# Kernel tuning notes

Hardware: AMD Instinct MI355X
Metric: run time of the kernel (lower is better)

The kernel has to match this reference:

```python
import jax, jax.numpy as jnp
import numpy as np

B, T, N, IN = 16, 12, 2048, 1
HID, E_DIM, CHEB, HOR = 64, 10, 2, 12


def setup_inputs() -> dict:
    key = jax.random.key(0)
    ks = jax.random.split(key, 12)
    s = 0.1  # param scale to keep gates unsaturated
    return {
        "source": jax.random.normal(ks[0], (B, T, N, IN), jnp.float32),
        "node_embeddings": jax.random.normal(ks[1], (N, E_DIM), jnp.float32),
        "Wg0": jax.random.normal(ks[2], (E_DIM, CHEB, IN + HID, 2 * HID), jnp.float32) * s,
        "bg0": jax.random.normal(ks[3], (E_DIM, 2 * HID), jnp.float32) * s,
        "Wu0": jax.random.normal(ks[4], (E_DIM, CHEB, IN + HID, HID), jnp.float32) * s,
        "bu0": jax.random.normal(ks[5], (E_DIM, HID), jnp.float32) * s,
        "Wg1": jax.random.normal(ks[6], (E_DIM, CHEB, HID + HID, 2 * HID), jnp.float32) * s,
        "bg1": jax.random.normal(ks[7], (E_DIM, 2 * HID), jnp.float32) * s,
        "Wu1": jax.random.normal(ks[8], (E_DIM, CHEB, HID + HID, HID), jnp.float32) * s,
        "bu1": jax.random.normal(ks[9], (E_DIM, HID), jnp.float32) * s,
        "conv_w": jax.random.normal(ks[10], (HOR, HID), jnp.float32) * s,
        "conv_b": jax.random.normal(ks[11], (HOR,), jnp.float32) * s,
    }


def _cheb_supports(E, cheb_k):
    # softmax(relu(E E^T)) row-normalized adaptive adjacency + Chebyshev recursion
    S = jax.nn.softmax(jax.nn.relu(E @ E.T), axis=1)
    sup = [jnp.eye(E.shape[0], dtype=S.dtype), S]
    for _ in range(2, cheb_k):
        sup.append(2.0 * S @ sup[-1] - sup[-2])
    return jnp.stack(sup, axis=0)  # (K, N, N)


def _gcn(x, supports, weights, bias):
    # x: (B,N,C); weights: (N,K,C,O); bias: (N,O)
    x_g = jnp.einsum('knm,bmc->bnkc', supports, x)
    return jnp.einsum('bnki,nkio->bno', x_g, weights) + bias


def _layer(x_seq, supports, E, Wg, bg, Wu, bu, hid):
    # precompute node-adaptive weights/biases (constant across time)
    wg = jnp.einsum('nd,dkio->nkio', E, Wg)
    bgv = E @ bg
    wu = jnp.einsum('nd,dkio->nkio', E, Wu)
    buv = E @ bu

    def step(state, x_t):
        inp = jnp.concatenate([x_t, state], axis=-1)
        zr = jax.nn.sigmoid(_gcn(inp, supports, wg, bgv))
        z, r = jnp.split(zr, 2, axis=-1)
        cand = jnp.concatenate([x_t, z * state], axis=-1)
        hc = jnp.tanh(_gcn(cand, supports, wu, buv))
        h = r * state + (1.0 - r) * hc
        return h, h

    init = jnp.zeros((x_seq.shape[0], x_seq.shape[2], hid), dtype=x_seq.dtype)
    _, hs = jax.lax.scan(step, init, jnp.swapaxes(x_seq, 0, 1))  # (T,B,N,H)
    return jnp.swapaxes(hs, 0, 1)  # (B,T,N,H)


def reference(source, node_embeddings, Wg0, bg0, Wu0, bu0, Wg1, bg1, Wu1, bu1, conv_w, conv_b):
    supports = _cheb_supports(node_embeddings, CHEB)
    h1 = _layer(source, supports, node_embeddings, Wg0, bg0, Wu0, bu0, HID)
    h2 = _layer(h1, supports, node_embeddings, Wg1, bg1, Wu1, bu1, HID)
    last = h2[:, -1]  # (B,N,HID)
    # Conv2d(1, horizon, kernel=(1,HID)) on (B,1,N,HID) == per-node linear over HID
    out = jnp.einsum('bnc,hc->bhn', last, conv_w) + conv_b[None, :, None]
    return out  # (B, horizon, N)
```

## Files before the change

kernel.cpp:

```cpp
#include <hip/hip_runtime.h>
#include <hip/hip_bf16.h>


#define B_    16
#define T_    12
#define N_    2048
#define HID_  64
#define ED_   10
#define HOR_  12
#define BH    (B_*HID_)
#define BT    (B_*T_)

typedef __hip_bfloat16 bf16;
typedef __attribute__((ext_vector_type(8))) short short8;
typedef __attribute__((ext_vector_type(4))) float floatx4;

__device__ __forceinline__ float b2f(bf16 x){ return __bfloat162float(x); }
__device__ __forceinline__ bf16  f2b(float x){ return __float2bfloat16(x); }
__device__ __forceinline__ float bits2f(unsigned u) {
  union { float f; unsigned i; } c; c.i = u << 16; return c.f;
}
__device__ __forceinline__ float ldin(const void* p, size_t i, int isbf) {
  return isbf ? b2f(((const bf16*)p)[i]) : ((const float*)p)[i];
}
__device__ __forceinline__ void fma4(float4& a, float s, const float4& b) {
  a.x += s*b.x; a.y += s*b.y; a.z += s*b.z; a.w += s*b.w;
}

__global__ void k_detect(const void* __restrict__ E, int* __restrict__ flag) {
  __shared__ int cnt;
  if (threadIdx.x == 0) cnt = 0;
  __syncthreads();
  const unsigned* w = (const unsigned*)E;
  int c = 0;
  for (int i = threadIdx.x; i < 4096; i += 256) {
    const unsigned e = (w[i] >> 7) & 0xFFu;
    if (e >= 0x6Eu && e <= 0x86u) ++c;
  }
  atomicAdd(&cnt, c);
  __syncthreads();
  if (threadIdx.x == 0) flag[0] = (cnt > 2048) ? 1 : 0;
}

__global__ void k_castE(const void* __restrict__ E, float* __restrict__ Ein,
                        const int* __restrict__ flag) {
  const int i = blockIdx.x*256 + threadIdx.x;
  if (i < N_*ED_) Ein[i] = ldin(E, i, flag[0]);
}
__global__ void k_castsrc(const void* __restrict__ src, float* __restrict__ srcf,
                          const int* __restrict__ flag) {
  const int i = blockIdx.x*256 + threadIdx.x;
  if (i < B_*T_*N_) srcf[i] = ldin(src, i, flag[0]);
}
__global__ void k_castc(const void* __restrict__ cw, const void* __restrict__ cb,
                        float* __restrict__ cwf, float* __restrict__ cbf,
                        const int* __restrict__ flag) {
  const int i = blockIdx.x*256 + threadIdx.x;
  const int f = flag[0];
  if (i < HOR_*HID_) cwf[i] = ldin(cw, i, f);
  if (i < HOR_)      cbf[i] = ldin(cb, i, f);
}

__global__ __launch_bounds__(256) void k_softmax_S(const float* __restrict__ Ein,
                                                   float* __restrict__ S) {
  const int n = blockIdx.x, tid = threadIdx.x;
  __shared__ float er[ED_];
  __shared__ float red[4];
  if (tid < ED_) er[tid] = Ein[n*ED_ + tid];
  __syncthreads();
  float e[ED_];
#pragma unroll
  for (int d = 0; d < ED_; ++d) e[d] = er[d];
  float v[8];
  float mx = 0.f;
#pragma unroll
  for (int j = 0; j < 8; ++j) {
    const int m = tid + j*256;
    float dot = 0.f;
#pragma unroll
    for (int d = 0; d < ED_; ++d) dot += e[d]*Ein[m*ED_ + d];
    v[j] = fmaxf(dot, 0.f);
    mx = fmaxf(mx, v[j]);
  }
  for (int o = 32; o; o >>= 1) mx = fmaxf(mx, __shfl_xor(mx, o, 64));
  if ((tid & 63) == 0) red[tid >> 6] = mx;
  __syncthreads();
  mx = fmaxf(fmaxf(red[0], red[1]), fmaxf(red[2], red[3]));
  __syncthreads();
  float sum = 0.f;
#pragma unroll
  for (int j = 0; j < 8; ++j) { v[j] = __expf(v[j] - mx); sum += v[j]; }
  for (int o = 32; o; o >>= 1) sum += __shfl_xor(sum, o, 64);
  if ((tid & 63) == 0) red[tid >> 6] = sum;
  __syncthreads();
  sum = red[0] + red[1] + red[2] + red[3];
  const float inv = 1.f / sum;
#pragma unroll
  for (int j = 0; j < 8; ++j)
    S[(size_t)n*N_ + tid + j*256] = v[j]*inv;
}

__global__ void k_splitS(const float* __restrict__ S, bf16* __restrict__ Sh,
                         bf16* __restrict__ Sl, int n) {
  const int i = blockIdx.x*256 + threadIdx.x;
  if (i < n) {
    const float v = S[i];
    const bf16 h = f2b(v);
    Sh[i] = h;
    Sl[i] = f2b(v - b2f(h));
  }
}

template<int LAYER>
__global__ __launch_bounds__(256) void k_prepP(const void* __restrict__ Wb,
                                               float* __restrict__ PF,
                                               bf16* __restrict__ PH,
                                               int KIin, int KIP, int O,
                                               const int* __restrict__ flag) {
  const int idx = blockIdx.x*256 + threadIdx.x;
  if (idx >= ED_*O*KIP) return;
  const int d = idx / (O*KIP), rem = idx - d*O*KIP;
  const int o = rem / KIP, kp = rem - o*KIP;
  int cheb, i; bool valid;
  if (LAYER == 0) {
    cheb = (kp >= 80) ? 1 : 0;
    const int local = kp - cheb*80;
    if (local < 64)       { i = local + 1; valid = true; }
    else if (local == 64) { i = 0;         valid = true; }
    else                  { i = 0;         valid = false; }
  } else {
    cheb = kp >> 7; i = kp & 127; valid = true;
  }
  float v = 0.f;
  if (valid) v = ldin(Wb, (size_t)((d*2 + cheb)*KIin + i)*O + o, flag[0]);
  const int kg = kp >> 2, e = kp & 3;
  const size_t pi = ((size_t)(o*(KIP/4) + kg)*ED_ + d)*4 + e;
  PF[pi] = v;
  PH[pi] = f2b(v);
}

__global__ __launch_bounds__(128) void k_matb(const float* __restrict__ Ein,
                                              const void* __restrict__ bb,
                                              float* __restrict__ outv, int O,
                                              const int* __restrict__ flag) {
  const int n = blockIdx.x, tid = threadIdx.x;
  if (tid >= O) return;
  const int f = flag[0];
  float acc = 0.f;
#pragma unroll
  for (int d = 0; d < ED_; ++d) acc += Ein[n*ED_ + d]*ldin(bb, d*O + tid, f);
  outv[n*O + tid] = acc;
}

__global__ __launch_bounds__(256) void k_gemm64T(const float* __restrict__ S,
                                                 const float* __restrict__ X,
                                                 float* __restrict__ C,
                                                 int ldx, int ldc) {
  const int bm = blockIdx.x * 64;
  const int bc = blockIdx.y * 64;
  __shared__ float St[64][68];
  __shared__ float Xt[64][68];
  const int tid = threadIdx.x;
  const int r0 = (tid >> 4) * 4;
  const int c0 = (tid & 15) * 4;
  float acc[4][4];
#pragma unroll
  for (int i = 0; i < 4; ++i)
#pragma unroll
    for (int j = 0; j < 4; ++j) acc[i][j] = 0.f;
  for (int mk = 0; mk < N_; mk += 64) {
    {
      const int r = tid >> 2, ks = (tid & 3) * 16;
      const float* sp = S + (size_t)(bm + r)*N_ + mk + ks;
#pragma unroll
      for (int u = 0; u < 16; ++u) St[ks + u][r] = sp[u];
      const float* xp = X + (size_t)(bc + r)*ldx + mk + ks;
#pragma unroll
      for (int u = 0; u < 16; ++u) Xt[ks + u][r] = xp[u];
    }
    __syncthreads();
#pragma unroll 4
    for (int kk = 0; kk < 64; ++kk) {
      const float a0 = St[kk][r0], a1 = St[kk][r0+1],
                  a2 = St[kk][r0+2], a3 = St[kk][r0+3];
      const float b0 = Xt[kk][c0], b1 = Xt[kk][c0+1],
                  b2 = Xt[kk][c0+2], b3 = Xt[kk][c0+3];
      acc[0][0] += a0*b0; acc[0][1] += a0*b1; acc[0][2] += a0*b2; acc[0][3] += a0*b3;
      acc[1][0] += a1*b0; acc[1][1] += a1*b1; acc[1][2] += a1*b2; acc[1][3] += a1*b3;
      acc[2][0] += a2*b0; acc[2][1] += a2*b1; acc[2][2] += a2*b2; acc[2][3] += a2*b3;
      acc[3][0] += a3*b0; acc[3][1] += a3*b1; acc[3][2] += a3*b2; acc[3][3] += a3*b3;
    }
    __syncthreads();
  }
#pragma unroll
  for (int i = 0; i < 4; ++i)
#pragma unroll
    for (int j = 0; j < 4; ++j)
      C[(size_t)(bm + r0 + i)*ldc + bc + c0 + j] = acc[i][j];
}

__global__ __launch_bounds__(256) void k_gemmM(const bf16* __restrict__ Sh,
                                               const bf16* __restrict__ Sl,
                                               const bf16* __restrict__ X1h,
                                               const bf16* __restrict__ X1l,
                                               float* __restrict__ C1, int ldc1,
                                               const bf16* __restrict__ X2h,
                                               const bf16* __restrict__ X2l,
                                               float* __restrict__ C2, int ldc2,
                                               int split) {
  const int bm = blockIdx.x * 128;
  int bc = blockIdx.y * 64;
  const bf16* Xh = X1h; const bf16* Xl = X1l; float* C = C1; int ldc = ldc1;
  if (bc >= split) { Xh = X2h; Xl = X2l; C = C2; ldc = ldc2; bc -= split; }

  __shared__ __align__(16) bf16 Ah[128][72];
  __shared__ __align__(16) bf16 Al[128][72];
  __shared__ __align__(16) bf16 Bh[64][72];
  __shared__ __align__(16) bf16 Bl[64][72];
  const int tid = threadIdx.x;
  const int wave = tid >> 6, lane = tid & 63, q = lane >> 4, ln = lane & 15;
  const int wm = wave >> 1, wn = wave & 1;
  const int srow = tid >> 3, scol = (tid & 7) * 8;

  floatx4 acc[4][2];
#pragma unroll
  for (int mt = 0; mt < 4; ++mt)
#pragma unroll
    for (int nt = 0; nt < 2; ++nt) acc[mt][nt] = (floatx4){0.f,0.f,0.f,0.f};

  for (int mk = 0; mk < N_; mk += 64) {
#pragma unroll
    for (int i = 0; i < 4; ++i) {
      const int r = i*32 + srow;
      *(uint4*)&Ah[r][scol] = *(const uint4*)(Sh + (size_t)(bm + r)*N_ + mk + scol);
      *(uint4*)&Al[r][scol] = *(const uint4*)(Sl + (size_t)(bm + r)*N_ + mk + scol);
    }
#pragma unroll
    for (int i = 0; i < 2; ++i) {
      const int r = i*32 + srow;
      *(uint4*)&Bh[r][scol] = *(const uint4*)(Xh + (size_t)(bc + r)*N_ + mk + scol);
      *(uint4*)&Bl[r][scol] = *(const uint4*)(Xl + (size_t)(bc + r)*N_ + mk + scol);
    }
    __syncthreads();
#pragma unroll
    for (int ks = 0; ks < 64; ks += 32) {
      short8 ah[4], al[4], bh[2], bl[2];
#pragma unroll
      for (int mt = 0; mt < 4; ++mt) {
        ah[mt] = *(const short8*)&Ah[wm*64 + mt*16 + ln][ks + q*8];
        al[mt] = *(const short8*)&Al[wm*64 + mt*16 + ln][ks + q*8];
      }
#pragma unroll
      for (int nt = 0; nt < 2; ++nt) {
        bh[nt] = *(const short8*)&Bh[wn*32 + nt*16 + ln][ks + q*8];
        bl[nt] = *(const short8*)&Bl[wn*32 + nt*16 + ln][ks + q*8];
      }
#pragma unroll
      for (int mt = 0; mt < 4; ++mt)
#pragma unroll
        for (int nt = 0; nt < 2; ++nt) {
          acc[mt][nt] = __builtin_amdgcn_mfma_f32_16x16x32_bf16(ah[mt], bh[nt], acc[mt][nt], 0, 0, 0);
          acc[mt][nt] = __builtin_amdgcn_mfma_f32_16x16x32_bf16(al[mt], bh[nt], acc[mt][nt], 0, 0, 0);
          acc[mt][nt] = __builtin_amdgcn_mfma_f32_16x16x32_bf16(ah[mt], bl[nt], acc[mt][nt], 0, 0, 0);
        }
    }
    __syncthreads();
  }
#pragma unroll
  for (int mt = 0; mt < 4; ++mt)
#pragma unroll
    for (int nt = 0; nt < 2; ++nt)
#pragma unroll
      for (int r = 0; r < 4; ++r)
        C[(size_t)(bm + wm*64 + mt*16 + q*4 + r)*ldc + bc + wn*32 + nt*16 + ln] =
            acc[mt][nt][r];
}

template<int LAYER, int KIP, int KIPP>
__device__ __forceinline__ void build4(float (*xg)[KIPP],
                                       const float* p0, const float* p1,
                                       const float* p2, const float* p3,
                                       int n, int t, int tid) {
  constexpr int NQ = KIP/4;
  for (int idx = tid; idx < B_*NQ; idx += 256) {
    const int b = idx / NQ, k = (idx - b*NQ) * 4;
    float4 v = make_float4(0.f, 0.f, 0.f, 0.f);
    if (LAYER == 1) {
      const float* rg = (k < 64) ? p0 : (k < 128) ? p1 : (k < 192) ? p2 : p3;
      v = *(const float4*)(rg + (size_t)n*BH + b*64 + (k & 63));
    } else {
      if (k < 64)        v = *(const float4*)(p0 + (size_t)n*BH + b*64 + k);
      else if (k == 64)  v.x = p1[(size_t)(b*T_ + t)*N_ + n];
      else if (k >= 80 && k < 144)
                         v = *(const float4*)(p2 + (size_t)n*BH + b*64 + (k - 80));
      else if (k == 144) v.x = p3[(size_t)n*BT + b*T_ + t];
    }
    *(float4*)&xg[b][k] = v;
  }
}

template<int KIP>
__device__ __forceinline__ float4 merge_p(const float* __restrict__ PF,
                                          const bf16* __restrict__ PH,
                                          const float* el, int o, int kg,
                                          int isbf) {
  float4 a4 = make_float4(0.f, 0.f, 0.f, 0.f);
  const size_t gbase = (size_t)(o*(KIP/4) + kg)*(ED_*4);
  if (isbf) {
    const uint4* g = (const uint4*)(PH + gbase);
#pragma unroll
    for (int i = 0; i < 5; ++i) {
      const uint4 w = g[i];
      const float e0 = el[2*i], e1 = el[2*i + 1];
      a4.x += e0*bits2f(w.x & 0xFFFFu); a4.y += e0*bits2f(w.x >> 16);
      a4.z += e0*bits2f(w.y & 0xFFFFu); a4.w += e0*bits2f(w.y >> 16);
      a4.x += e1*bits2f(w.z & 0xFFFFu); a4.y += e1*bits2f(w.z >> 16);
      a4.z += e1*bits2f(w.w & 0xFFFFu); a4.w += e1*bits2f(w.w >> 16);
    }
  } else {
    const float4* g = (const float4*)(PF + gbase);
#pragma unroll
    for (int d = 0; d < ED_; ++d)
      fma4(a4, el[d], g[d]);
  }
  return a4;
}

template<int KIP>
__device__ __forceinline__ void merge_p2(const float* __restrict__ PF,
                                         const bf16* __restrict__ PH,
                                         const float* el0, const float* el1,
                                         int o, int kg, int isbf,
                                         float4& a0, float4& a1) {
  const size_t gbase = (size_t)(o*(KIP/4) + kg)*(ED_*4);
  if (isbf) {
    const uint4* g = (const uint4*)(PH + gbase);
#pragma unroll
    for (int i = 0; i < 5; ++i) {
      const uint4 w = g[i];
      const float f0 = bits2f(w.x & 0xFFFFu), f1 = bits2f(w.x >> 16);
      const float f2 = bits2f(w.y & 0xFFFFu), f3 = bits2f(w.y >> 16);
      const float f4 = bits2f(w.z & 0xFFFFu), f5 = bits2f(w.z >> 16);
      const float f6 = bits2f(w.w & 0xFFFFu), f7 = bits2f(w.w >> 16);
      const float e00 = el0[2*i], e01 = el0[2*i + 1];
      const float e10 = el1[2*i], e11 = el1[2*i + 1];
      a0.x += e00*f0; a0.y += e00*f1; a0.z += e00*f2; a0.w += e00*f3;
      a0.x += e01*f4; a0.y += e01*f5; a0.z += e01*f6; a0.w += e01*f7;
      a1.x += e10*f0; a1.y += e10*f1; a1.z += e10*f2; a1.w += e10*f3;
      a1.x += e11*f4; a1.y += e11*f5; a1.z += e11*f6; a1.w += e11*f7;
    }
  } else {
    const float4* g = (const float4*)(PF + gbase);
#pragma unroll
    for (int d = 0; d < ED_; ++d) {
      const float4 w = g[d];
      fma4(a0, el0[d], w);
      fma4(a1, el1[d], w);
    }
  }
}

template<int KIP>
__global__ __launch_bounds__(256) void k_merge(const float* __restrict__ PF,
                                               const bf16* __restrict__ PH,
                                               const float* __restrict__ Ein,
                                               float* __restrict__ WM, int O,
                                               const int* __restrict__ flag) {
  const int n = blockIdx.x;
  const int idx = blockIdx.y*256 + threadIdx.x;
  __shared__ float es[ED_];
  if (threadIdx.x < ED_) es[threadIdx.x] = Ein[n*ED_ + threadIdx.x];
  __syncthreads();
  if (idx >= O*(KIP/4)) return;
  const int o = idx / (KIP/4), kg = idx - o*(KIP/4);
  float el[ED_];
#pragma unroll
  for (int d = 0; d < ED_; ++d) el[d] = es[d];
  const float4 a4 = merge_p<KIP>(PF, PH, el, o, kg, flag[0]);
  *(float4*)&WM[((size_t)n*O + o)*KIP + kg*4] = a4;
}

template<int LAYER, int KIP>
__global__ __launch_bounds__(256, 2) void k_gateWpm(const float* __restrict__ WM,
                                                    const float* __restrict__ bgv,
                                                    const float* __restrict__ p0,
                                                    const float* __restrict__ p1,
                                                    const float* __restrict__ p2,
                                                    const float* __restrict__ p3,
                                                    const float* __restrict__ hstate,
                                                    float* __restrict__ zh,
                                                    bf16* __restrict__ zhTh,
                                                    bf16* __restrict__ zhTl,
                                                    float* __restrict__ r_buf,
                                                    int t) {
  constexpr int KIPP = KIP + 4;
  constexpr int O = 128;
  const int n = blockIdx.x, tid = threadIdx.x;
  __shared__ float xg[B_][KIPP];
  __shared__ float wm[O][36];
  build4<LAYER, KIP, KIPP>(xg, p0, p1, p2, p3, n, t, tid);

  const float* WMn = WM + (size_t)n*O*KIP;
  const int b = tid >> 4, q = tid & 15;
  float acc[8];
#pragma unroll
  for (int j = 0; j < 8; ++j) acc[j] = 0.f;

  for (int k0 = 0; k0 < KIP; k0 += 32) {
#pragma unroll
    for (int i = 0; i < O*8/256; ++i) {
      const int idx = tid + i*256;
      const int o = idx >> 3, kq = idx & 7;
      *(float4*)&wm[o][kq*4] =
          *(const float4*)(WMn + (size_t)o*KIP + k0 + kq*4);
    }
    __syncthreads();
#pragma unroll
    for (int kq = 0; kq < 8; ++kq) {
      const float4 xv = *(const float4*)&xg[b][k0 + kq*4];
#pragma unroll
      for (int j = 0; j < 8; ++j) {
        const float4 wv = *(const float4*)&wm[q + 16*j][kq*4];
        acc[j] += xv.x*wv.x + xv.y*wv.y + xv.z*wv.z + xv.w*wv.w;
      }
    }
    __syncthreads();
  }
#pragma unroll
  for (int j = 0; j < 8; ++j) {
    const int o = q + 16*j;
    float s = acc[j] + bgv[n*128 + o];
    s = 1.f/(1.f + __expf(-s));
    if (o < HID_) {
      const float zv = s*hstate[(size_t)n*BH + b*64 + o];
      zh[(size_t)n*BH + b*64 + o] = zv;
      const bf16 h = f2b(zv);
      zhTh[(size_t)(b*64 + o)*N_ + n] = h;
      zhTl[(size_t)(b*64 + o)*N_ + n] = f2b(zv - b2f(h));
    } else {
      r_buf[(size_t)n*BH + b*64 + (o - HID_)] = s;
    }
  }
}

template<int LAYER, int KIP>
__global__ __launch_bounds__(256, 2) void k_candWpm(const float* __restrict__ WM,
                                                    const float* __restrict__ buv,
                                                    const float* __restrict__ p0,
                                                    const float* __restrict__ p1,
                                                    const float* __restrict__ p2,
                                                    const float* __restrict__ p3,
                                                    const float* __restrict__ r_buf,
                                                    float* __restrict__ hstate,
                                                    bf16* __restrict__ hTh,
                                                    bf16* __restrict__ hTl,
                                                    int t) {
  constexpr int KIPP = KIP + 4;
  constexpr int O = 64;
  const int n = blockIdx.x, tid = threadIdx.x;
  __shared__ float xg[B_][KIPP];
  __shared__ float wm[O][36];
  build4<LAYER, KIP, KIPP>(xg, p0, p1, p2, p3, n, t, tid);

  const float* WMn = WM + (size_t)n*O*KIP;
  const int b = tid >> 4, q = tid & 15;
  float acc[4];
#pragma unroll
  for (int j = 0; j < 4; ++j) acc[j] = 0.f;

  for (int k0 = 0; k0 < KIP; k0 += 32) {
#pragma unroll
    for (int i = 0; i < O*8/256; ++i) {
      const int idx = tid + i*256;
      const int o = idx >> 3, kq = idx & 7;
      *(float4*)&wm[o][kq*4] =
          *(const float4*)(WMn + (size_t)o*KIP + k0 + kq*4);
    }
    __syncthreads();
#pragma unroll
    for (int kq = 0; kq < 8; ++kq) {
      const float4 xv = *(const float4*)&xg[b][k0 + kq*4];
#pragma unroll
      for (int j = 0; j < 4; ++j) {
        const float4 wv = *(const float4*)&wm[q + 16*j][kq*4];
        acc[j] += xv.x*wv.x + xv.y*wv.y + xv.z*wv.z + xv.w*wv.w;
      }
    }
    __syncthreads();
  }
#pragma unroll
  for (int j = 0; j < 4; ++j) {
    const int o = q + 16*j;
    const float hc = tanhf(acc[j] + buv[n*64 + o]);
    const float rr = r_buf[(size_t)n*BH + b*64 + o];
    const float hold = hstate[(size_t)n*BH + b*64 + o];
    const float hn = rr*hold + (1.f - rr)*hc;
    hstate[(size_t)n*BH + b*64 + o] = hn;
    const bf16 h = f2b(hn);
    hTh[(size_t)(b*64 + o)*N_ + n] = h;
    hTl[(size_t)(b*64 + o)*N_ + n] = f2b(hn - b2f(h));
  }
}

template<int LAYER, int KIP>
__global__ __launch_bounds__(256) void k_gateW(const float* __restrict__ PF,
                                               const bf16* __restrict__ PH,
                                               const float* __restrict__ bgv,
                                               const float* __restrict__ p0,
                                               const float* __restrict__ p1,
                                               const float* __restrict__ p2,
                                               const float* __restrict__ p3,
                                               const float* __restrict__ Ein,
                                               const float* __restrict__ hstate,
                                               float* __restrict__ zh,
                                               bf16* __restrict__ zhTh,
                                               bf16* __restrict__ zhTl,
                                               float* __restrict__ r_buf,
                                               const int* __restrict__ flag,
                                               int t) {
  constexpr int KIPP = KIP + 4;
  constexpr int O = 128;
  const int n = blockIdx.x, tid = threadIdx.x;
  __shared__ float xg[B_][KIPP];
  __shared__ float wm[O][36];
  __shared__ float es[ED_];
  if (tid < ED_) es[tid] = Ein[n*ED_ + tid];
  build4<LAYER, KIP, KIPP>(xg, p0, p1, p2, p3, n, t, tid);
  __syncthreads();
  const int isbf = flag[0];
  float el[ED_];
#pragma unroll
  for (int d = 0; d < ED_; ++d) el[d] = es[d];

  const int b = tid >> 4, q = tid & 15;
  float acc[8];
#pragma unroll
  for (int j = 0; j < 8; ++j) acc[j] = 0.f;

  for (int k0 = 0; k0 < KIP; k0 += 32) {
#pragma unroll
    for (int i = 0; i < O*8/256; ++i) {
      const int idx = tid + i*256;
      const int o = idx >> 3, kq = idx & 7;
      const float4 a4 = merge_p<KIP>(PF, PH, el, o, (k0 >> 2) + kq, isbf);
      *(float4*)&wm[o][kq*4] = a4;
    }
    __syncthreads();
#pragma unroll
    for (int kq = 0; kq < 8; ++kq) {
      const float4 xv = *(const float4*)&xg[b][k0 + kq*4];
#pragma unroll
      for (int j = 0; j < 8; ++j) {
        const float4 wv = *(const float4*)&wm[q + 16*j][kq*4];
        acc[j] += xv.x*wv.x + xv.y*wv.y + xv.z*wv.z + xv.w*wv.w;
      }
    }
    __syncthreads();
  }
#pragma unroll
  for (int j = 0; j < 8; ++j) {
    const int o = q + 16*j;
    float s = acc[j] + bgv[n*128 + o];
    s = 1.f/(1.f + __expf(-s));
    if (o < HID_) {
      const float zv = s*hstate[(size_t)n*BH + b*64 + o];
      zh[(size_t)n*BH + b*64 + o] = zv;
      const bf16 h = f2b(zv);
      zhTh[(size_t)(b*64 + o)*N_ + n] = h;
      zhTl[(size_t)(b*64 + o)*N_ + n] = f2b(zv - b2f(h));
    } else {
      r_buf[(size_t)n*BH + b*64 + (o - HID_)] = s;
    }
  }
}

template<int LAYER, int KIP>
__global__ __launch_bounds__(256, 2) void k_gateW2(const float* __restrict__ PF,
                                                   const bf16* __restrict__ PH,
                                                   const float* __restrict__ bgv,
                                                   const float* __restrict__ p0,
                                                   const float* __restrict__ p1,
                                                   const float* __restrict__ p2,
                                                   const float* __restrict__ p3,
                                                   const float* __restrict__ Ein,
                                                   const float* __restrict__ hstate,
                                                   float* __restrict__ zh,
                                                   bf16* __restrict__ zhTh,
                                                   bf16* __restrict__ zhTl,
                                                   float* __restrict__ r_buf,
                                                   const int* __restrict__ flag,
                                                   int t) {
  constexpr int KIPP = KIP + 4;
  constexpr int O = 128;
  const int n0 = blockIdx.x, n1 = blockIdx.x + N_/2, tid = threadIdx.x;
  __shared__ float xg[2][B_][KIPP];
  __shared__ float wm[2][O][36];
  __shared__ float es[2][ED_];
  if (tid < ED_) es[0][tid] = Ein[n0*ED_ + tid];
  if (tid >= 32 && tid < 32 + ED_) es[1][tid - 32] = Ein[n1*ED_ + (tid - 32)];
  build4<LAYER, KIP, KIPP>(xg[0], p0, p1, p2, p3, n0, t, tid);
  build4<LAYER, KIP, KIPP>(xg[1], p0, p1, p2, p3, n1, t, tid);
  __syncthreads();
  const int isbf = flag[0];
  float el0[ED_], el1[ED_];
#pragma unroll
  for (int d = 0; d < ED_; ++d) { el0[d] = es[0][d]; el1[d] = es[1][d]; }

  const int b = tid >> 4, q = tid & 15;
  float ac0[8], ac1[8];
#pragma unroll
  for (int j = 0; j < 8; ++j) { ac0[j] = 0.f; ac1[j] = 0.f; }

  for (int k0 = 0; k0 < KIP; k0 += 32) {
#pragma unroll
    for (int i = 0; i < O*8/256; ++i) {
      const int idx = tid + i*256;
      const int o = idx >> 3, kq = idx & 7;
      float4 a0 = make_float4(0.f, 0.f, 0.f, 0.f);
      float4 a1 = make_float4(0.f, 0.f, 0.f, 0.f);
      merge_p2<KIP>(PF, PH, el0, el1, o, (k0 >> 2) + kq, isbf, a0, a1);
      *(float4*)&wm[0][o][kq*4] = a0;
      *(float4*)&wm[1][o][kq*4] = a1;
    }
    __syncthreads();
#pragma unroll
    for (int kq = 0; kq < 8; ++kq) {
      const float4 xv0 = *(const float4*)&xg[0][b][k0 + kq*4];
      const float4 xv1 = *(const float4*)&xg[1][b][k0 + kq*4];
#pragma unroll
      for (int j = 0; j < 8; ++j) {
        const float4 w0 = *(const float4*)&wm[0][q + 16*j][kq*4];
        const float4 w1 = *(const float4*)&wm[1][q + 16*j][kq*4];
        ac0[j] += xv0.x*w0.x + xv0.y*w0.y + xv0.z*w0.z + xv0.w*w0.w;
        ac1[j] += xv1.x*w1.x + xv1.y*w1.y + xv1.z*w1.z + xv1.w*w1.w;
      }
    }
    __syncthreads();
  }
#pragma unroll
  for (int j = 0; j < 8; ++j) {
    const int o = q + 16*j;
    {
      float s = ac0[j] + bgv[n0*128 + o];
      s = 1.f/(1.f + __expf(-s));
      if (o < HID_) {
        const float zv = s*hstate[(size_t)n0*BH + b*64 + o];
        zh[(size_t)n0*BH + b*64 + o] = zv;
        const bf16 h = f2b(zv);
        zhTh[(size_t)(b*64 + o)*N_ + n0] = h;
        zhTl[(size_t)(b*64 + o)*N_ + n0] = f2b(zv - b2f(h));
      } else {
        r_buf[(size_t)n0*BH + b*64 + (o - HID_)] = s;
      }
    }
    {
      float s = ac1[j] + bgv[n1*128 + o];
      s = 1.f/(1.f + __expf(-s));
      if (o < HID_) {
        const float zv = s*hstate[(size_t)n1*BH + b*64 + o];
        zh[(size_t)n1*BH + b*64 + o] = zv;
        const bf16 h = f2b(zv);
        zhTh[(size_t)(b*64 + o)*N_ + n1] = h;
        zhTl[(size_t)(b*64 + o)*N_ + n1] = f2b(zv - b2f(h));
      } else {
        r_buf[(size_t)n1*BH + b*64 + (o - HID_)] = s;
      }
    }
  }
}

template<int LAYER, int KIP>
__global__ __launch_bounds__(256) void k_candW(const float* __restrict__ PF,
                                               const bf16* __restrict__ PH,
                                               const float* __restrict__ buv,
                                               const float* __restrict__ p0,
                                               const float* __restrict__ p1,
                                               const float* __restrict__ p2,
                                               const float* __restrict__ p3,
                                               const float* __restrict__ Ein,
                                               const float* __restrict__ r_buf,
                                               float* __restrict__ hstate,
                                               bf16* __restrict__ hTh,
                                               bf16* __restrict__ hTl,
                                               const int* __restrict__ flag,
                                               int t) {
  constexpr int KIPP = KIP + 4;
  constexpr int O = 64;
  const int n = blockIdx.x, tid = threadIdx.x;
  __shared__ float xg[B_][KIPP];
  __shared__ float wm[O][36];
  __shared__ float es[ED_];
  if (tid < ED_) es[tid] = Ein[n*ED_ + tid];
  build4<LAYER, KIP, KIPP>(xg, p0, p1, p2, p3, n, t, tid);
  __syncthreads();
  const int isbf = flag[0];
  float el[ED_];
#pragma unroll
  for (int d = 0; d < ED_; ++d) el[d] = es[d];

  const int b = tid >> 4, q = tid & 15;
  float acc[4];
#pragma unroll
  for (int j = 0; j < 4; ++j) acc[j] = 0.f;

  for (int k0 = 0; k0 < KIP; k0 += 32) {
#pragma unroll
    for (int i = 0; i < O*8/256; ++i) {
      const int idx = tid + i*256;
      const int o = idx >> 3, kq = idx & 7;
      const float4 a4 = merge_p<KIP>(PF, PH, el, o, (k0 >> 2) + kq, isbf);
      *(float4*)&wm[o][kq*4] = a4;
    }
    __syncthreads();
#pragma unroll
    for (int kq = 0; kq < 8; ++kq) {
      const float4 xv = *(const float4*)&xg[b][k0 + kq*4];
#pragma unroll
      for (int j = 0; j < 4; ++j) {
        const float4 wv = *(const float4*)&wm[q + 16*j][kq*4];
        acc[j] += xv.x*wv.x + xv.y*wv.y + xv.z*wv.z + xv.w*wv.w;
      }
    }
    __syncthreads();
  }
#pragma unroll
  for (int j = 0; j < 4; ++j) {
    const int o = q + 16*j;
    const float hc = tanhf(acc[j] + buv[n*64 + o]);
    const float rr = r_buf[(size_t)n*BH + b*64 + o];
    const float hold = hstate[(size_t)n*BH + b*64 + o];
    const float hn = rr*hold + (1.f - rr)*hc;
    hstate[(size_t)n*BH + b*64 + o] = hn;
    const bf16 h = f2b(hn);
    hTh[(size_t)(b*64 + o)*N_ + n] = h;
    hTl[(size_t)(b*64 + o)*N_ + n] = f2b(hn - b2f(h));
  }
}

__global__ void k_zero_f(float* __restrict__ p, int n) {
  const int i = blockIdx.x*256 + threadIdx.x;
  if (i < n) p[i] = 0.f;
}
__global__ void k_zero_out(void* __restrict__ out, int nelem,
                           const int* __restrict__ flag) {
  const int i = blockIdx.x*256 + threadIdx.x;
  if (i < nelem) {
    if (flag[0]) ((unsigned short*)out)[i] = 0;
    else         ((float*)out)[i] = 0.f;
  }
}

__global__ __launch_bounds__(256) void k_conv(const float* __restrict__ h2,
                                              const float* __restrict__ cwf,
                                              const float* __restrict__ cbf,
                                              void* __restrict__ out,
                                              const int* __restrict__ flag) {
  const int n = blockIdx.x, tid = threadIdx.x;
  __shared__ float hs[BH];
  for (int i = tid; i < BH; i += 256) hs[i] = h2[(size_t)n*BH + i];
  __syncthreads();
  const int isbf = flag[0];
  for (int i = tid; i < B_*HOR_; i += 256) {
    const int b = i / HOR_, hor = i - b*HOR_;
    float acc = cbf[hor];
#pragma unroll
    for (int c = 0; c < HID_; ++c) acc += hs[b*HID_ + c]*cwf[hor*HID_ + c];
    const size_t oi = (size_t)(b*HOR_ + hor)*N_ + n;
    if (isbf) ((bf16*)out)[oi] = f2b(acc);
    else      ((float*)out)[oi] = acc;
  }
}

extern "C" void kernel_launch(void* const* d_in, const int* in_sizes, int n_in,
                              void* d_out, int out_size, void* d_ws, size_t ws_size,
                              hipStream_t stream) {
  const void* src = d_in[0];
  const void* E   = d_in[1];
  const void* Wg0 = d_in[2];
  const void* bg0 = d_in[3];
  const void* Wu0 = d_in[4];
  const void* bu0 = d_in[5];
  const void* Wg1 = d_in[6];
  const void* bg1 = d_in[7];
  const void* Wu1 = d_in[8];
  const void* bu1 = d_in[9];
  const void* cw  = d_in[10];
  const void* cb  = d_in[11];
  (void)in_sizes; (void)n_in;

  char* p = (char*)d_ws;
  char* ws_end = (char*)d_ws + ws_size;
  auto alloc = [&](size_t bytes) -> char* {
    char* r = p; p += (bytes + 255) & ~(size_t)255; return r;
  };
  const size_t SL = (size_t)N_*BH;
  int*   flag  = (int*)  alloc(256);
  float* Ein   = (float*)alloc((size_t)N_*ED_*4);
  float* cwf   = (float*)alloc((size_t)HOR_*HID_*4);
  float* cbf   = (float*)alloc((size_t)HOR_*4);
  float* S_f   = (float*)alloc((size_t)N_*N_*4);
  bf16*  S_hi  = (bf16*) alloc((size_t)N_*N_*2);
  bf16*  S_lo  = (bf16*) alloc((size_t)N_*N_*2);
  float* Wg0F  = (float*)alloc((size_t)ED_*128*160*4);
  float* Wu0F  = (float*)alloc((size_t)ED_*64*160*4);
  float* Wg1F  = (float*)alloc((size_t)ED_*128*256*4);
  float* Wu1F  = (float*)alloc((size_t)ED_*64*256*4);
  bf16*  Wg0H  = (bf16*) alloc((size_t)ED_*128*160*2);
  bf16*  Wu0H  = (bf16*) alloc((size_t)ED_*64*160*2);
  bf16*  Wg1H  = (bf16*) alloc((size_t)ED_*128*256*2);
  bf16*  Wu1H  = (bf16*) alloc((size_t)ED_*64*256*2);
  float* bgv0  = (float*)alloc((size_t)N_*128*4);
  float* buv0  = (float*)alloc((size_t)N_*64*4);
  float* bgv1  = (float*)alloc((size_t)N_*128*4);
  float* buv1  = (float*)alloc((size_t)N_*64*4);
  float* srcf  = (float*)alloc((size_t)BT*N_*4);
  float* Sx0   = (float*)alloc((size_t)N_*BT*4);
  float* h0    = (float*)alloc(SL*4);
  float* h2    = (float*)alloc(SL*4);
  float* Sh_a  = (float*)alloc(SL*4);
  float* Sh_b  = (float*)alloc(SL*4);
  float* zh    = (float*)alloc(SL*4);
  float* r_buf = (float*)alloc(SL*4);
  bf16*  zhTh  = (bf16*) alloc(SL*2);
  bf16*  zhTl  = (bf16*) alloc(SL*2);
  bf16*  h0Th  = (bf16*) alloc(SL*2);
  bf16*  h0Tl  = (bf16*) alloc(SL*2);
  bf16*  h2Th  = (bf16*) alloc(SL*2);
  bf16*  h2Tl  = (bf16*) alloc(SL*2);

  const size_t required_base = (size_t)(p - (char*)d_ws);

  float* Wu0M = (float*)alloc((size_t)N_*64*160*4);   bool pmWu0 = (p <= ws_end);
  float* Wu1M = (float*)alloc((size_t)N_*64*256*4);   bool pmWu1 = (p <= ws_end);
  float* Wg0M = (float*)alloc((size_t)N_*128*160*4);  bool pmWg0 = (p <= ws_end);
  float* Wg1M = (float*)alloc((size_t)N_*128*256*4);  bool pmWg1 = (p <= ws_end);

  auto cdiv = [](int a, int b) { return (a + b - 1) / b; };

  k_detect<<<dim3(1), 256, 0, stream>>>(E, flag);

  if (required_base > ws_size) {
    k_zero_out<<<dim3(cdiv(out_size, 256)), 256, 0, stream>>>(d_out, out_size, flag);
    return;
  }

  k_castE  <<<dim3(cdiv(N_*ED_, 256)), 256, 0, stream>>>(E, Ein, flag);
  k_castsrc<<<dim3(cdiv(BT*N_, 256)),  256, 0, stream>>>(src, srcf, flag);
  k_castc  <<<dim3(cdiv(HOR_*HID_, 256)), 256, 0, stream>>>(cw, cb, cwf, cbf, flag);
  k_prepP<0><<<dim3(cdiv(ED_*128*160, 256)), 256, 0, stream>>>(Wg0, Wg0F, Wg0H, 65, 160, 128, flag);
  k_prepP<0><<<dim3(cdiv(ED_*64*160,  256)), 256, 0, stream>>>(Wu0, Wu0F, Wu0H, 65, 160, 64, flag);
  k_prepP<1><<<dim3(cdiv(ED_*128*256, 256)), 256, 0, stream>>>(Wg1, Wg1F, Wg1H, 128, 256, 128, flag);
  k_prepP<1><<<dim3(cdiv(ED_*64*256,  256)), 256, 0, stream>>>(Wu1, Wu1F, Wu1H, 128, 256, 64, flag);
  k_matb<<<dim3(N_), 128, 0, stream>>>(Ein, bg0, bgv0, 128, flag);
  k_matb<<<dim3(N_), 128, 0, stream>>>(Ein, bu0, buv0, 64,  flag);
  k_matb<<<dim3(N_), 128, 0, stream>>>(Ein, bg1, bgv1, 128, flag);
  k_matb<<<dim3(N_), 128, 0, stream>>>(Ein, bu1, buv1, 64,  flag);
  k_softmax_S<<<dim3(N_), 256, 0, stream>>>(Ein, S_f);
  k_splitS<<<dim3(cdiv(N_*N_, 256)), 256, 0, stream>>>(S_f, S_hi, S_lo, N_*N_);

  if (pmWu0) k_merge<160><<<dim3(N_, 10), 256, 0, stream>>>(Wu0F, Wu0H, Ein, Wu0M, 64,  flag);
  if (pmWu1) k_merge<256><<<dim3(N_, 16), 256, 0, stream>>>(Wu1F, Wu1H, Ein, Wu1M, 64,  flag);
  if (pmWg0) k_merge<160><<<dim3(N_, 20), 256, 0, stream>>>(Wg0F, Wg0H, Ein, Wg0M, 128, flag);
  if (pmWg1) k_merge<256><<<dim3(N_, 32), 256, 0, stream>>>(Wg1F, Wg1H, Ein, Wg1M, 128, flag);

  k_gemm64T<<<dim3(N_/64, BT/64), 256, 0, stream>>>(S_f, srcf, Sx0, N_, BT);

  k_zero_f<<<dim3((int)((2*SL + 255)/256)), 256, 0, stream>>>(h0, (int)(2*SL));
  k_zero_f<<<dim3((int)((2*SL + 255)/256)), 256, 0, stream>>>(Sh_a, (int)(2*SL));

  auto run_gate0 = [&](int t) {
    if (pmWg0)
      k_gateWpm<0,160><<<dim3(N_), 256, 0, stream>>>(Wg0M, bgv0, h0, srcf, Sh_a, Sx0,
                                                     h0, zh, zhTh, zhTl, r_buf, t);
    else
      k_gateW2<0,160><<<dim3(N_/2), 256, 0, stream>>>(Wg0F, Wg0H, bgv0, h0, srcf, Sh_a, Sx0,
                                                      Ein, h0, zh, zhTh, zhTl, r_buf, flag, t);
  };
  auto run_cand0 = [&](int t) {
    if (pmWu0)
      k_candWpm<0,160><<<dim3(N_), 256, 0, stream>>>(Wu0M, buv0, zh, srcf, Sh_b, Sx0,
                                                     r_buf, h0, h0Th, h0Tl, t);
    else
      k_candW<0,160><<<dim3(N_), 256, 0, stream>>>(Wu0F, Wu0H, buv0, zh, srcf, Sh_b, Sx0,
                                                   Ein, r_buf, h0, h0Th, h0Tl, flag, t);
  };
  auto run_gate1 = [&](int t) {
    if (pmWg1)
      k_gateWpm<1,256><<<dim3(N_), 256, 0, stream>>>(Wg1M, bgv1, h0, h2, Sh_a, Sh_b,
                                                     h2, zh, zhTh, zhTl, r_buf, t);
    else
      k_gateW2<1,256><<<dim3(N_/2), 256, 0, stream>>>(Wg1F, Wg1H, bgv1, h0, h2, Sh_a, Sh_b,
                                                      Ein, h2, zh, zhTh, zhTl, r_buf, flag, t);
  };
  auto run_cand1 = [&](int t) {
    if (pmWu1)
      k_candWpm<1,256><<<dim3(N_), 256, 0, stream>>>(Wu1M, buv1, h0, zh, Sh_a, Sh_b,
                                                     r_buf, h2, h2Th, h2Tl, t);
    else
      k_candW<1,256><<<dim3(N_), 256, 0, stream>>>(Wu1F, Wu1H, buv1, h0, zh, Sh_a, Sh_b,
                                                   Ein, r_buf, h2, h2Th, h2Tl, flag, t);
  };

  run_gate0(0);
  run_cand0(0);
  k_gemmM<<<dim3(N_/128, BH/64), 256, 0, stream>>>(S_hi, S_lo, h0Th, h0Tl, Sh_a, BH,
                                                   h0Th, h0Tl, Sh_a, BH, 1 << 30);
  run_gate1(0);
  run_cand1(0);

  for (int t = 1; t < T_; ++t) {
    run_gate0(t);
    k_gemmM<<<dim3(N_/128, BH/64), 256, 0, stream>>>(S_hi, S_lo, zhTh, zhTl, Sh_b, BH,
                                                     zhTh, zhTl, Sh_b, BH, 1 << 30);
    run_cand0(t);
    k_gemmM<<<dim3(N_/128, 2*BH/64), 256, 0, stream>>>(S_hi, S_lo, h0Th, h0Tl, Sh_a, BH,
                                                       h2Th, h2Tl, Sh_b, BH, BH);
    run_gate1(t);
    k_gemmM<<<dim3(N_/128, BH/64), 256, 0, stream>>>(S_hi, S_lo, zhTh, zhTl, Sh_b, BH,
                                                     zhTh, zhTl, Sh_b, BH, 1 << 30);
    run_cand1(t);
  }

  k_conv<<<dim3(N_), 256, 0, stream>>>(h2, cwf, cbf, d_out, flag);
}
```

Baseline: 6.559 ms.

## Process two nodes per block in candidate kernel and stream input chunks

The candidate kernel now handles two nodes per block, like the gate kernel already does, so each weight-basis load in merge_p2 serves both nodes. Both kernels now load the input activations one 32-wide chunk at a time into a small shared buffer instead of building the full row up front. Launch bounds move from 2 to 3 blocks per SM. The aim is less shared memory and more occupancy, at the cost of more register pressure and an input load inside every chunk iteration.

```diff
diff --git a/kernel.cpp b/kernel.cpp
--- a/kernel.cpp
+++ b/kernel.cpp
@@ -299,6 +299,24 @@
   }
 }
 
+template<int LAYER>
+__device__ __forceinline__ float4 xchunk_load(const float* p0, const float* p1,
+                                              const float* p2, const float* p3,
+                                              int n, int t, int b, int k) {
+  float4 v = make_float4(0.f, 0.f, 0.f, 0.f);
+  if (LAYER == 1) {
+    const float* rg = (k < 64) ? p0 : (k < 128) ? p1 : (k < 192) ? p2 : p3;
+    v = *(const float4*)(rg + (size_t)n*BH + b*64 + (k & 63));
+  } else {
+    if (k < 64)        v = *(const float4*)(p0 + (size_t)n*BH + b*64 + k);
+    else if (k == 64)  v.x = p1[(size_t)(b*T_ + t)*N_ + n];
+    else if (k >= 80 && k < 144)
+                       v = *(const float4*)(p2 + (size_t)n*BH + b*64 + (k - 80));
+    else if (k == 144) v.x = p3[(size_t)n*BT + b*T_ + t];
+  }
+  return v;
+}
+
 template<int KIP>
 __device__ __forceinline__ float4 merge_p(const float* __restrict__ PF,
                                           const bf16* __restrict__ PH,
@@ -503,79 +521,7 @@
 }
 
 template<int LAYER, int KIP>
-__global__ __launch_bounds__(256) void k_gateW(const float* __restrict__ PF,
-                                               const bf16* __restrict__ PH,
-                                               const float* __restrict__ bgv,
-                                               const float* __restrict__ p0,
-                                               const float* __restrict__ p1,
-                                               const float* __restrict__ p2,
-                                               const float* __restrict__ p3,
-                                               const float* __restrict__ Ein,
-                                               const float* __restrict__ hstate,
-                                               float* __restrict__ zh,
-                                               bf16* __restrict__ zhTh,
-                                               bf16* __restrict__ zhTl,
-                                               float* __restrict__ r_buf,
-                                               const int* __restrict__ flag,
-                                               int t) {
-  constexpr int KIPP = KIP + 4;
-  constexpr int O = 128;
-  const int n = blockIdx.x, tid = threadIdx.x;
-  __shared__ float xg[B_][KIPP];
-  __shared__ float wm[O][36];
-  __shared__ float es[ED_];
-  if (tid < ED_) es[tid] = Ein[n*ED_ + tid];
-  build4<LAYER, KIP, KIPP>(xg, p0, p1, p2, p3, n, t, tid);
-  __syncthreads();
-  const int isbf = flag[0];
-  float el[ED_];
-#pragma unroll
-  for (int d = 0; d < ED_; ++d) el[d] = es[d];
-
-  const int b = tid >> 4, q = tid & 15;
-  float acc[8];
-#pragma unroll
-  for (int j = 0; j < 8; ++j) acc[j] = 0.f;
-
-  for (int k0 = 0; k0 < KIP; k0 += 32) {
-#pragma unroll
-    for (int i = 0; i < O*8/256; ++i) {
-      const int idx = tid + i*256;
-      const int o = idx >> 3, kq = idx & 7;
-      const float4 a4 = merge_p<KIP>(PF, PH, el, o, (k0 >> 2) + kq, isbf);
-      *(float4*)&wm[o][kq*4] = a4;
-    }
-    __syncthreads();
-#pragma unroll
-    for (int kq = 0; kq < 8; ++kq) {
-      const float4 xv = *(const float4*)&xg[b][k0 + kq*4];
-#pragma unroll
-      for (int j = 0; j < 8; ++j) {
-        const float4 wv = *(const float4*)&wm[q + 16*j][kq*4];
-        acc[j] += xv.x*wv.x + xv.y*wv.y + xv.z*wv.z + xv.w*wv.w;
-      }
-    }
-    __syncthreads();
-  }
-#pragma unroll
-  for (int j = 0; j < 8; ++j) {
-    const int o = q + 16*j;
-    float s = acc[j] + bgv[n*128 + o];
-    s = 1.f/(1.f + __expf(-s));
-    if (o < HID_) {
-      const float zv = s*hstate[(size_t)n*BH + b*64 + o];
-      zh[(size_t)n*BH + b*64 + o] = zv;
-      const bf16 h = f2b(zv);
-      zhTh[(size_t)(b*64 + o)*N_ + n] = h;
-      zhTl[(size_t)(b*64 + o)*N_ + n] = f2b(zv - b2f(h));
-    } else {
-      r_buf[(size_t)n*BH + b*64 + (o - HID_)] = s;
-    }
-  }
-}
-
-template<int LAYER, int KIP>
-__global__ __launch_bounds__(256, 2) void k_gateW2(const float* __restrict__ PF,
+__global__ __launch_bounds__(256, 3) void k_gateW2(const float* __restrict__ PF,
                                                    const bf16* __restrict__ PH,
                                                    const float* __restrict__ bgv,
                                                    const float* __restrict__ p0,
@@ -590,16 +536,13 @@
                                                    float* __restrict__ r_buf,
                                                    const int* __restrict__ flag,
                                                    int t) {
-  constexpr int KIPP = KIP + 4;
   constexpr int O = 128;
   const int n0 = blockIdx.x, n1 = blockIdx.x + N_/2, tid = threadIdx.x;
-  __shared__ float xg[2][B_][KIPP];
+  __shared__ float xgc[2][B_][36];
   __shared__ float wm[2][O][36];
   __shared__ float es[2][ED_];
   if (tid < ED_) es[0][tid] = Ein[n0*ED_ + tid];
   if (tid >= 32 && tid < 32 + ED_) es[1][tid - 32] = Ein[n1*ED_ + (tid - 32)];
-  build4<LAYER, KIP, KIPP>(xg[0], p0, p1, p2, p3, n0, t, tid);
-  build4<LAYER, KIP, KIPP>(xg[1], p0, p1, p2, p3, n1, t, tid);
   __syncthreads();
   const int isbf = flag[0];
   float el0[ED_], el1[ED_];
@@ -607,11 +550,14 @@
   for (int d = 0; d < ED_; ++d) { el0[d] = es[0][d]; el1[d] = es[1][d]; }
 
   const int b = tid >> 4, q = tid & 15;
+  const int snn = tid >> 7, sb = (tid >> 3) & 15, sk = tid & 7;
   float ac0[8], ac1[8];
 #pragma unroll
   for (int j = 0; j < 8; ++j) { ac0[j] = 0.f; ac1[j] = 0.f; }
 
   for (int k0 = 0; k0 < KIP; k0 += 32) {
+    *(float4*)&xgc[snn][sb][sk*4] =
+        xchunk_load<LAYER>(p0, p1, p2, p3, snn ? n1 : n0, t, sb, k0 + sk*4);
 #pragma unroll
     for (int i = 0; i < O*8/256; ++i) {
       const int idx = tid + i*256;
@@ -625,8 +571,8 @@
     __syncthreads();
 #pragma unroll
     for (int kq = 0; kq < 8; ++kq) {
-      const float4 xv0 = *(const float4*)&xg[0][b][k0 + kq*4];
-      const float4 xv1 = *(const float4*)&xg[1][b][k0 + kq*4];
+      const float4 xv0 = *(const float4*)&xgc[0][b][kq*4];
+      const float4 xv1 = *(const float4*)&xgc[1][b][kq*4];
 #pragma unroll
       for (int j = 0; j < 8; ++j) {
         const float4 w0 = *(const float4*)&wm[0][q + 16*j][kq*4];
@@ -670,55 +616,63 @@
 }
 
 template<int LAYER, int KIP>
-__global__ __launch_bounds__(256) void k_candW(const float* __restrict__ PF,
-                                               const bf16* __restrict__ PH,
-                                               const float* __restrict__ buv,
-                                               const float* __restrict__ p0,
-                                               const float* __restrict__ p1,
-                                               const float* __restrict__ p2,
-                                               const float* __restrict__ p3,
-                                               const float* __restrict__ Ein,
-                                               const float* __restrict__ r_buf,
-                                               float* __restrict__ hstate,
-                                               bf16* __restrict__ hTh,
-                                               bf16* __restrict__ hTl,
-                                               const int* __restrict__ flag,
-                                               int t) {
-  constexpr int KIPP = KIP + 4;
+__global__ __launch_bounds__(256, 3) void k_candW2(const float* __restrict__ PF,
+                                                   const bf16* __restrict__ PH,
+                                                   const float* __restrict__ buv,
+                                                   const float* __restrict__ p0,
+                                                   const float* __restrict__ p1,
+                                                   const float* __restrict__ p2,
+                                                   const float* __restrict__ p3,
+                                                   const float* __restrict__ Ein,
+                                                   const float* __restrict__ r_buf,
+                                                   float* __restrict__ hstate,
+                                                   bf16* __restrict__ hTh,
+                                                   bf16* __restrict__ hTl,
+                                                   const int* __restrict__ flag,
+                                                   int t) {
   constexpr int O = 64;
-  const int n = blockIdx.x, tid = threadIdx.x;
-  __shared__ float xg[B_][KIPP];
-  __shared__ float wm[O][36];
-  __shared__ float es[ED_];
-  if (tid < ED_) es[tid] = Ein[n*ED_ + tid];
-  build4<LAYER, KIP, KIPP>(xg, p0, p1, p2, p3, n, t, tid);
+  const int n0 = blockIdx.x, n1 = blockIdx.x + N_/2, tid = threadIdx.x;
+  __shared__ float xgc[2][B_][36];
+  __shared__ float wm[2][O][36];
+  __shared__ float es[2][ED_];
+  if (tid < ED_) es[0][tid] = Ein[n0*ED_ + tid];
+  if (tid >= 32 && tid < 32 + ED_) es[1][tid - 32] = Ein[n1*ED_ + (tid - 32)];
   __syncthreads();
   const int isbf = flag[0];
-  float el[ED_];
-#pragma unroll
-  for (int d = 0; d < ED_; ++d) el[d] = es[d];
+  float el0[ED_], el1[ED_];
+#pragma unroll
+  for (int d = 0; d < ED_; ++d) { el0[d] = es[0][d]; el1[d] = es[1][d]; }
 
   const int b = tid >> 4, q = tid & 15;
-  float acc[4];
-#pragma unroll
-  for (int j = 0; j < 4; ++j) acc[j] = 0.f;
+  const int snn = tid >> 7, sb = (tid >> 3) & 15, sk = tid & 7;
+  float ac0[4], ac1[4];
+#pragma unroll
+  for (int j = 0; j < 4; ++j) { ac0[j] = 0.f; ac1[j] = 0.f; }
 
   for (int k0 = 0; k0 < KIP; k0 += 32) {
+    *(float4*)&xgc[snn][sb][sk*4] =
+        xchunk_load<LAYER>(p0, p1, p2, p3, snn ? n1 : n0, t, sb, k0 + sk*4);
 #pragma unroll
     for (int i = 0; i < O*8/256; ++i) {
       const int idx = tid + i*256;
       const int o = idx >> 3, kq = idx & 7;
-      const float4 a4 = merge_p<KIP>(PF, PH, el, o, (k0 >> 2) + kq, isbf);
-      *(float4*)&wm[o][kq*4] = a4;
+      float4 a0 = make_float4(0.f, 0.f, 0.f, 0.f);
+      float4 a1 = make_float4(0.f, 0.f, 0.f, 0.f);
+      merge_p2<KIP>(PF, PH, el0, el1, o, (k0 >> 2) + kq, isbf, a0, a1);
+      *(float4*)&wm[0][o][kq*4] = a0;
+      *(float4*)&wm[1][o][kq*4] = a1;
     }
     __syncthreads();
 #pragma unroll
     for (int kq = 0; kq < 8; ++kq) {
-      const float4 xv = *(const float4*)&xg[b][k0 + kq*4];
+      const float4 xv0 = *(const float4*)&xgc[0][b][kq*4];
+      const float4 xv1 = *(const float4*)&xgc[1][b][kq*4];
 #pragma unroll
       for (int j = 0; j < 4; ++j) {
-        const float4 wv = *(const float4*)&wm[q + 16*j][kq*4];
-        acc[j] += xv.x*wv.x + xv.y*wv.y + xv.z*wv.z + xv.w*wv.w;
+        const float4 w0 = *(const float4*)&wm[0][q + 16*j][kq*4];
+        const float4 w1 = *(const float4*)&wm[1][q + 16*j][kq*4];
+        ac0[j] += xv0.x*w0.x + xv0.y*w0.y + xv0.z*w0.z + xv0.w*w0.w;
+        ac1[j] += xv1.x*w1.x + xv1.y*w1.y + xv1.z*w1.z + xv1.w*w1.w;
       }
     }
     __syncthreads();
@@ -726,14 +680,26 @@
 #pragma unroll
   for (int j = 0; j < 4; ++j) {
     const int o = q + 16*j;
-    const float hc = tanhf(acc[j] + buv[n*64 + o]);
-    const float rr = r_buf[(size_t)n*BH + b*64 + o];
-    const float hold = hstate[(size_t)n*BH + b*64 + o];
-    const float hn = rr*hold + (1.f - rr)*hc;
-    hstate[(size_t)n*BH + b*64 + o] = hn;
-    const bf16 h = f2b(hn);
-    hTh[(size_t)(b*64 + o)*N_ + n] = h;
-    hTl[(size_t)(b*64 + o)*N_ + n] = f2b(hn - b2f(h));
+    {
+      const float hc = tanhf(ac0[j] + buv[n0*64 + o]);
+      const float rr = r_buf[(size_t)n0*BH + b*64 + o];
+      const float hold = hstate[(size_t)n0*BH + b*64 + o];
+      const float hn = rr*hold + (1.f - rr)*hc;
+      hstate[(size_t)n0*BH + b*64 + o] = hn;
+      const bf16 h = f2b(hn);
+      hTh[(size_t)(b*64 + o)*N_ + n0] = h;
+      hTl[(size_t)(b*64 + o)*N_ + n0] = f2b(hn - b2f(h));
+    }
+    {
+      const float hc = tanhf(ac1[j] + buv[n1*64 + o]);
+      const float rr = r_buf[(size_t)n1*BH + b*64 + o];
+      const float hold = hstate[(size_t)n1*BH + b*64 + o];
+      const float hn = rr*hold + (1.f - rr)*hc;
+      hstate[(size_t)n1*BH + b*64 + o] = hn;
+      const bf16 h = f2b(hn);
+      hTh[(size_t)(b*64 + o)*N_ + n1] = h;
+      hTl[(size_t)(b*64 + o)*N_ + n1] = f2b(hn - b2f(h));
+    }
   }
 }
 
@@ -881,8 +847,8 @@
       k_candWpm<0,160><<<dim3(N_), 256, 0, stream>>>(Wu0M, buv0, zh, srcf, Sh_b, Sx0,
                                                      r_buf, h0, h0Th, h0Tl, t);
     else
-      k_candW<0,160><<<dim3(N_), 256, 0, stream>>>(Wu0F, Wu0H, buv0, zh, srcf, Sh_b, Sx0,
-                                                   Ein, r_buf, h0, h0Th, h0Tl, flag, t);
+      k_candW2<0,160><<<dim3(N_/2), 256, 0, stream>>>(Wu0F, Wu0H, buv0, zh, srcf, Sh_b, Sx0,
+                                                      Ein, r_buf, h0, h0Th, h0Tl, flag, t);
   };
   auto run_gate1 = [&](int t) {
     if (pmWg1)
@@ -897,8 +863,8 @@
       k_candWpm<1,256><<<dim3(N_), 256, 0, stream>>>(Wu1M, buv1, h0, zh, Sh_a, Sh_b,
                                                      r_buf, h2, h2Th, h2Tl, t);
     else
-      k_candW<1,256><<<dim3(N_), 256, 0, stream>>>(Wu1F, Wu1H, buv1, h0, zh, Sh_a, Sh_b,
-                                                   Ein, r_buf, h2, h2Th, h2Tl, flag, t);
+      k_candW2<1,256><<<dim3(N_/2), 256, 0, stream>>>(Wu1F, Wu1H, buv1, h0, zh, Sh_a, Sh_b,
+                                                      Ein, r_buf, h2, h2Th, h2Tl, flag, t);
   };
 
   run_gate0(0);
```

Result: slower. 6.951 ms (+6.0%).
